# Performance work log

Hardware: AMD Instinct MI355X
Metric: run time of the kernel (lower is better)

Reference implementation:

```python
import jax, jax.numpy as jnp
import numpy as np

# static config (matches init_kwargs)
DIM = 192; NUM_HEAD = 6; HEAD_DIM = DIM // NUM_HEAD
WIN = 8; WS = WIN * WIN            # win_seq = 64
B = 2; H = 256; Wd = 256
RH = H // WIN; RW = Wd // WIN; L = RH * RW   # 32x32 = 1024 windows
P = (2 * WIN - 1) ** 2             # 225 relative positions
SCALE = HEAD_DIM ** -0.5


def _relative_index():
    # same math as get_relative_index (torch.meshgrid default = 'ij')
    coords = np.stack(np.meshgrid(np.arange(WIN), np.arange(WIN), indexing='ij'))
    cf = coords.reshape(2, -1)
    rel = (cf[:, :, None] - cf[:, None, :]).transpose(1, 2, 0).copy()
    rel[:, :, 0] += WIN - 1
    rel[:, :, 1] += WIN - 1
    rel[:, :, 0] *= 2 * WIN - 1
    return rel.sum(-1).reshape(-1)  # (WS*WS,), values in [0, P)

POS_INDEX = jnp.asarray(_relative_index())


def _table_nb(rh, rw):
    # reflect-pad(1) + 3x3 unfold of window-id table -> neighbor window ids (L, 9)
    t = np.arange(rh * rw).reshape(rh, rw)
    tp = np.pad(t, 1, mode='reflect')
    nb = np.stack([tp[kh:kh + rh, kw:kw + rw] for kh in range(3) for kw in range(3)], axis=-1)
    return nb.reshape(rh * rw, 9)

TABLE_NB = jnp.asarray(_table_nb(RH, RW))  # (L, 9) int


def _unfold9(x):
    # x: (B, C, rh, rw) -> (B, L, C, 9); reflect pad 1 + 3x3 neighborhoods
    rh, rw = x.shape[2], x.shape[3]
    xp = jnp.pad(x, ((0, 0), (0, 0), (1, 1), (1, 1)), mode='reflect')
    nb = jnp.stack([xp[:, :, kh:kh + rh, kw:kw + rw] for kh in range(3) for kw in range(3)], axis=-1)
    return nb.reshape(x.shape[0], x.shape[1], rh * rw, 9).transpose(0, 2, 1, 3)


def _router(q, k, pos_embedding):
    # router runs on detached q, k (q.detach() in source)
    qd = jax.lax.stop_gradient(q)
    kd = jax.lax.stop_gradient(k)
    qr = qd.reshape(B, DIM, RH, WIN, RW, WIN).mean(axis=(3, 5))
    kr = kd.reshape(B, DIM, RH, WIN, RW, WIN).mean(axis=(3, 5))
    qr_flat = qr.reshape(B, DIM, L).transpose(0, 2, 1)      # (B, L, C)
    kr_fold = _unfold9(kr)                                   # (B, L, C, 9)
    a_r = jnp.einsum('blc,blcn->bln', qr_flat, kr_fold)      # routing scores
    a_r = a_r.at[..., 4].add(-100.0)                          # exclude self window
    # softmax is monotone -> argmax of a_r equals argmax of softmax(a_r)
    idx = jnp.argmax(a_r, axis=-1)                            # (B, L) in [0,9)
    idx_reflect = TABLE_NB[jnp.arange(L)[None, :], idx]       # (B, L) routed window id
    itself = pos_embedding[4]                                 # (nh, P)
    dirb = pos_embedding[idx]                                 # (B, L, nh, P)
    itself_b = itself[:, POS_INDEX].reshape(NUM_HEAD, WS, WS)
    itself_b = jnp.broadcast_to(itself_b, (B, L, NUM_HEAD, WS, WS))
    dir_b = dirb[..., POS_INDEX].reshape(B, L, NUM_HEAD, WS, WS)
    pos_embed = jnp.concatenate([itself_b, dir_b], axis=-1)   # (B, L, nh, WS, 2*WS)
    return idx_reflect, pos_embed


def reference(x, pos_embedding):
    # x: (B, 3*DIM, H, W) fused qkv feature map
    qc = x[:, :DIM]
    kc = x[:, DIM:2 * DIM]
    idx, pos_embed = _router(qc, kc, pos_embedding)
    # winP: window partition into (3, B, L, nh, WS, hd)
    qkv = x.reshape(B, 3, NUM_HEAD, HEAD_DIM, RH, WIN, RW, WIN)
    qkv = qkv.transpose(1, 0, 4, 6, 2, 5, 7, 3).reshape(3, B, L, NUM_HEAD, WS, HEAD_DIM)
    q, k, v = qkv[0], qkv[1], qkv[2]
    gather = jax.vmap(lambda a, i: a[i])     # per-batch window gather along L
    k_d = gather(k, idx)                     # (B, L, nh, WS, hd)
    v_d = gather(v, idx)
    k_g = jnp.concatenate([k, k_d], axis=3)  # (B, L, nh, 2*WS, hd)
    v_g = jnp.concatenate([v, v_d], axis=3)
    attn = jnp.einsum('blhsd,blhtd->blhst', q, k_g) * SCALE + pos_embed
    attn = jax.nn.softmax(attn, axis=-1)
    out = jnp.einsum('blhst,blhtd->blhsd', attn, v_g)  # (B, L, nh, WS, hd)
    # winR: window reverse to (B, DIM, H, W)
    out = out.reshape(B, RH, RW, NUM_HEAD, WIN, WIN, HEAD_DIM)
    out = out.transpose(0, 3, 6, 1, 4, 2, 5).reshape(B, DIM, H, Wd)
    return out


def setup_inputs() -> dict:
    key = jax.random.key(0)
    k1, k2 = jax.random.split(key)
    x = jax.random.normal(k1, (B, 3 * DIM, H, Wd), dtype=jnp.float32)
    pos_embedding = jax.random.normal(k2, (9, NUM_HEAD, P), dtype=jnp.float32) * 0.02
    return {"x": x, "pos_embedding": pos_embedding}
```

## Files before the change

### kernel.cpp

```cpp
#include <hip/hip_runtime.h>
#include <math.h>

namespace {
constexpr int cB   = 2;
constexpr int cDIM = 192;
constexpr int cNH  = 6;
constexpr int cHD  = 32;
constexpr int cH   = 256;
constexpr int cW   = 256;
constexpr int cRH  = 32;
constexpr int cL   = 1024;
constexpr int cP   = 225;
constexpr float cSCALE = 0.17677669529663688f;
}

typedef _Float16 h8 __attribute__((ext_vector_type(8)));
typedef _Float16 h4 __attribute__((ext_vector_type(4)));
typedef float    f4 __attribute__((ext_vector_type(4)));

__global__ void pool_kernel(const float* __restrict__ x, float* __restrict__ pool) {
    int blk = blockIdx.x;
    int rh = blk & 31;
    int c  = (blk >> 5) % 384;
    int b  = blk / (384 * 32);
    int tid = threadIdx.x;
    int i  = tid >> 5;
    int rw = tid & 31;
    const float* row = x + (((size_t)(b * 576 + c)) * cH + rh * 8 + i) * cW + rw * 8;
    float4 a0 = *(const float4*)row;
    float4 a1 = *(const float4*)(row + 4);
    float s = a0.x + a0.y + a0.z + a0.w + a1.x + a1.y + a1.z + a1.w;
    __shared__ float red[8][33];
    red[i][rw] = s;
    __syncthreads();
    if (tid < 32) {
        float t = 0.f;
        #pragma unroll
        for (int k = 0; k < 8; ++k) t += red[k][tid];
        pool[((size_t)(b * cL) + rh * 32 + tid) * 384 + c] = t * (1.0f / 64.0f);
    }
}

__global__ void router_kernel(const float* __restrict__ pool, int* __restrict__ idxbuf) {
    int blk = blockIdx.x;
    int l = blk & (cL - 1);
    int b = blk >> 10;
    int rh = l >> 5, rw = l & 31;
    int lane = threadIdx.x;
    int ln[9];
    #pragma unroll
    for (int n = 0; n < 9; ++n) {
        int nh = rh + n / 3 - 1;
        int nw = rw + n % 3 - 1;
        nh = nh < 0 ? 1 : (nh > 31 ? 30 : nh);
        nw = nw < 0 ? 1 : (nw > 31 ? 30 : nw);
        ln[n] = nh * 32 + nw;
    }
    float acc[9] = {0,0,0,0,0,0,0,0,0};
    const float* qb = pool + ((size_t)(b * cL) + l) * 384;
    #pragma unroll
    for (int ci = 0; ci < 3; ++ci) {
        int c = lane + ci * 64;
        float q = qb[c];
        #pragma unroll
        for (int n = 0; n < 9; ++n)
            acc[n] += q * pool[((size_t)(b * cL) + ln[n]) * 384 + 192 + c];
    }
    #pragma unroll
    for (int n = 0; n < 9; ++n)
        #pragma unroll
        for (int off = 32; off > 0; off >>= 1)
            acc[n] += __shfl_down(acc[n], off);
    if (lane == 0) {
        acc[4] -= 100.0f;
        int bi = 0; float bv = acc[0];
        #pragma unroll
        for (int n = 1; n < 9; ++n) if (acc[n] > bv) { bv = acc[n]; bi = n; }
        idxbuf[blk * 2]     = bi;
        idxbuf[blk * 2 + 1] = ln[bi];
    }
}

__global__ __launch_bounds__(256, 3) void attn_kernel(
    const float* __restrict__ x, const float* __restrict__ pe,
    const int* __restrict__ idxbuf, float* __restrict__ out)
{
    __shared__ _Float16 Qh[64 * 40];
    __shared__ _Float16 Kh[128 * 40];
    __shared__ _Float16 Vt[32 * 136];
    __shared__ _Float16 Pst[4][16 * 136];
    __shared__ float    pes[2 * cP];

    int blk = blockIdx.x;
    int h  = blk >> 11;
    int bl = blk & 2047;
    int b  = bl >> 10;
    int l  = bl & 1023;
    int rh = l >> 5, rw = l & 31;
    int tid = threadIdx.x;

    int dir  = idxbuf[bl * 2];
    int lwin = idxbuf[bl * 2 + 1];
    int rh2 = lwin >> 5, rw2 = lwin & 31;

    const float* pe_self = pe + (4 * cNH + h) * cP;
    const float* pe_dir  = pe + (dir * cNH + h) * cP;
    for (int t = tid; t < 2 * cP; t += 256)
        pes[t] = (t < cP) ? pe_self[t] : pe_dir[t - cP];

    {
        int d = tid & 31;
        int i = tid >> 5;
        const size_t CHW = (size_t)cH * cW;
        const float* xb = x + (size_t)b * (3 * cDIM) * CHW;
        size_t off_self = (size_t)(rh  * 8 + i) * cW + rw  * 8;
        size_t off_dir  = (size_t)(rh2 * 8 + i) * cW + rw2 * 8;
        size_t cq = (size_t)(h * cHD + d) * CHW;
        size_t ck = cq + (size_t)cDIM * CHW;
        size_t cv = ck + (size_t)cDIM * CHW;

        {
            float4 a0 = *(const float4*)(xb + cq + off_self);
            float4 a1 = *(const float4*)(xb + cq + off_self + 4);
            float vv[8] = {a0.x,a0.y,a0.z,a0.w,a1.x,a1.y,a1.z,a1.w};
            #pragma unroll
            for (int j = 0; j < 8; ++j)
                Qh[(i * 8 + j) * 40 + d] = (_Float16)(vv[j] * cSCALE);
        }
        {
            float4 a0 = *(const float4*)(xb + ck + off_self);
            float4 a1 = *(const float4*)(xb + ck + off_self + 4);
            float vv[8] = {a0.x,a0.y,a0.z,a0.w,a1.x,a1.y,a1.z,a1.w};
            #pragma unroll
            for (int j = 0; j < 8; ++j)
                Kh[(i * 8 + j) * 40 + d] = (_Float16)vv[j];
            float4 b0 = *(const float4*)(xb + ck + off_dir);
            float4 b1 = *(const float4*)(xb + ck + off_dir + 4);
            float ww[8] = {b0.x,b0.y,b0.z,b0.w,b1.x,b1.y,b1.z,b1.w};
            #pragma unroll
            for (int j = 0; j < 8; ++j)
                Kh[(64 + i * 8 + j) * 40 + d] = (_Float16)ww[j];
        }
        {
            float4 a0 = *(const float4*)(xb + cv + off_self);
            float4 a1 = *(const float4*)(xb + cv + off_self + 4);
            h8 hv = { (_Float16)a0.x,(_Float16)a0.y,(_Float16)a0.z,(_Float16)a0.w,
                      (_Float16)a1.x,(_Float16)a1.y,(_Float16)a1.z,(_Float16)a1.w };
            *(h8*)&Vt[d * 136 + i * 8] = hv;
            float4 b0 = *(const float4*)(xb + cv + off_dir);
            float4 b1 = *(const float4*)(xb + cv + off_dir + 4);
            h8 hw = { (_Float16)b0.x,(_Float16)b0.y,(_Float16)b0.z,(_Float16)b0.w,
                      (_Float16)b1.x,(_Float16)b1.y,(_Float16)b1.z,(_Float16)b1.w };
            *(h8*)&Vt[d * 136 + 64 + i * 8] = hw;
        }
    }
    __syncthreads();

    int lane = tid & 63;
    int w    = tid >> 6;
    int g    = lane >> 4;
    int sl   = lane & 15;
    int s_global = w * 16 + sl;

    int base0 = ((s_global >> 3) + 7) * 15 + (s_global & 7) + 7;
    int offs[4];
    #pragma unroll
    for (int q = 0; q < 4; ++q) {
        int gq = 4 * g + q;
        offs[q] = (gq >> 3) * 15 + (gq & 7);
    }

    h8 qf = *(const h8*)&Qh[s_global * 40 + g * 8];
    f4 ST[8];
    #pragma unroll
    for (int T = 0; T < 8; ++T) {
        int base = ((T < 4) ? 0 : cP) + base0 - (T & 3) * 30;
        f4 c;
        #pragma unroll
        for (int q = 0; q < 4; ++q) c[q] = pes[base - offs[q]];
        h8 kf = *(const h8*)&Kh[(T * 16 + sl) * 40 + g * 8];
        ST[T] = __builtin_amdgcn_mfma_f32_16x16x32_f16(kf, qf, c, 0, 0, 0);
    }

    float mx = -1e30f;
    #pragma unroll
    for (int T = 0; T < 8; ++T)
        #pragma unroll
        for (int q = 0; q < 4; ++q) mx = fmaxf(mx, ST[T][q]);
    mx = fmaxf(mx, __shfl_xor(mx, 16));
    mx = fmaxf(mx, __shfl_xor(mx, 32));
    float sum = 0.f;
    #pragma unroll
    for (int T = 0; T < 8; ++T)
        #pragma unroll
        for (int q = 0; q < 4; ++q) { float e = __expf(ST[T][q] - mx); ST[T][q] = e; sum += e; }
    sum += __shfl_xor(sum, 16);
    sum += __shfl_xor(sum, 32);
    float r = 1.0f / sum;

    _Float16* prow = &Pst[w][sl * 136];
    #pragma unroll
    for (int T = 0; T < 8; ++T) {
        h4 p = { (_Float16)(ST[T][0] * r), (_Float16)(ST[T][1] * r),
                 (_Float16)(ST[T][2] * r), (_Float16)(ST[T][3] * r) };
        *(h4*)&prow[T * 16 + g * 4] = p;
    }

    f4 O0 = {0.f,0.f,0.f,0.f}, O1 = {0.f,0.f,0.f,0.f};
    #pragma unroll
    for (int kb = 0; kb < 4; ++kb) {
        h8 pf = *(const h8*)&Pst[w][sl * 136 + kb * 32 + g * 8];
        h8 v0 = *(const h8*)&Vt[ sl       * 136 + kb * 32 + g * 8];
        h8 v1 = *(const h8*)&Vt[(16 + sl) * 136 + kb * 32 + g * 8];
        O0 = __builtin_amdgcn_mfma_f32_16x16x32_f16(v0, pf, O0, 0, 0, 0);
        O1 = __builtin_amdgcn_mfma_f32_16x16x32_f16(v1, pf, O1, 0, 0, 0);
    }

    const size_t CHW = (size_t)cH * cW;
    int pr = rh * 8 + (s_global >> 3);
    int pc = rw * 8 + (s_global & 7);
    float* ob = out + ((size_t)(b * cDIM + h * cHD)) * CHW + (size_t)pr * cW + pc;
    #pragma unroll
    for (int q = 0; q < 4; ++q) {
        ob[(size_t)(4 * g + q) * CHW]      = O0[q];
        ob[(size_t)(16 + 4 * g + q) * CHW] = O1[q];
    }
}

extern "C" void kernel_launch(void* const* d_in, const int* in_sizes, int n_in,
                              void* d_out, int out_size, void* d_ws, size_t ws_size,
                              hipStream_t stream) {
    const float* x  = (const float*)d_in[0];
    const float* pe = (const float*)d_in[1];
    float* out = (float*)d_out;
    float* pool   = (float*)d_ws;
    int*   idxbuf = (int*)((char*)d_ws + (size_t)cB * cL * 384 * sizeof(float));

    hipLaunchKernelGGL(pool_kernel,   dim3(cB * 384 * cRH), dim3(256), 0, stream, x, pool);
    hipLaunchKernelGGL(router_kernel, dim3(cB * cL),        dim3(64),  0, stream, pool, idxbuf);
    hipLaunchKernelGGL(attn_kernel,   dim3(cNH * cB * cL),  dim3(256), 0, stream, x, pe, idxbuf, out);
}
```

Baseline: 610.8 us.

## Pre-transform Q/K/V into per-window fp16 layout fused with pooling

Adds a transform kernel that reads x once, computes the pooled q/k means, and writes Q (pre-scaled), K and V as fp16 in a contiguous per-window, per-head layout. The attention kernel then loads fragments straight from these buffers instead of gathering strided fp32 data from x and staging it in shared memory. This replaces the old separate pool pass and cuts redundant reads of x. The cost is an extra fp16 round trip through global memory of about 3x25MB and a larger workspace. The old path is kept as a fallback for when the workspace is too small.

```diff
diff --git a/kernel.cpp b/kernel.cpp
--- a/kernel.cpp
+++ b/kernel.cpp
@@ -17,6 +17,222 @@
 typedef _Float16 h8 __attribute__((ext_vector_type(8)));
 typedef _Float16 h4 __attribute__((ext_vector_type(4)));
 typedef float    f4 __attribute__((ext_vector_type(4)));
+
+
+__global__ __launch_bounds__(256, 6) void transform_kernel(
+    const float* __restrict__ x, float* __restrict__ pool,
+    _Float16* __restrict__ QT, _Float16* __restrict__ KT, _Float16* __restrict__ VT)
+{
+    __shared__ _Float16 Ls[4 * 64 * 40];
+
+    int blk = blockIdx.x;
+    int rw4 = blk & 7;
+    int rhh = (blk >> 3) & 31;
+    int r   = blk >> 8;
+    int h = r % 6; r /= 6;
+    int t = r % 3;
+    int b = r / 3;
+    int tid  = threadIdx.x;
+    int lane = tid & 63;
+    int hh   = lane >> 3;
+    int ww4  = lane & 7;
+    int c0   = t * cDIM + h * 32;
+    int l0   = rhh * 32 + rw4 * 4;
+
+    const size_t CHW = (size_t)cH * cW;
+    size_t vbase = ((size_t)(b * cNH + h) * cL) * 2048;
+
+    #pragma unroll
+    for (int k = 0; k < 8; ++k) {
+        int c = (tid >> 6) + 4 * k;
+        const float* src = x + ((size_t)(b * 3 * cDIM + c0 + c)) * CHW
+                         + (size_t)(rhh * 8 + hh) * cW + rw4 * 32 + ww4 * 4;
+        float4 v = *(const float4*)src;
+
+        if (t < 2) {
+            float ps = v.x + v.y + v.z + v.w;
+            ps += __shfl_xor(ps, 1);
+            ps += __shfl_xor(ps, 8);
+            ps += __shfl_xor(ps, 16);
+            ps += __shfl_xor(ps, 32);
+            if ((lane & 1) == 0 && lane < 8) {
+                int w = lane >> 1;
+                pool[((size_t)(b * cL) + l0 + w) * 384 + t * 192 + h * 32 + c] = ps * (1.0f / 64.0f);
+            }
+            float sc = (t == 0) ? cSCALE : 1.0f;
+            int ll = ww4 >> 1;
+            int s0 = hh * 8 + (ww4 & 1) * 4;
+            float vv[4] = {v.x, v.y, v.z, v.w};
+            #pragma unroll
+            for (int j = 0; j < 4; ++j)
+                Ls[(ll * 64 + s0 + j) * 40 + c] = (_Float16)(vv[j] * sc);
+        } else {
+            int ll = ww4 >> 1;
+            int tt = hh * 8 + (ww4 & 1) * 4;
+            h4 hv = { (_Float16)v.x, (_Float16)v.y, (_Float16)v.z, (_Float16)v.w };
+            *(h4*)&VT[vbase + (size_t)(l0 + ll) * 2048 + c * 64 + tt] = hv;
+        }
+    }
+
+    if (t < 2) {
+        __syncthreads();
+        _Float16* dst = (t == 0) ? QT : KT;
+        size_t obase = ((size_t)(b * cNH + h) * cL) * 2048;
+        #pragma unroll
+        for (int j = 0; j < 4; ++j) {
+            int linear = tid + 256 * j;
+            int ll = linear >> 8;
+            int s  = (linear >> 2) & 63;
+            int d8 = linear & 3;
+            h8 val = *(const h8*)&Ls[(ll * 64 + s) * 40 + d8 * 8];
+            *(h8*)&dst[obase + (size_t)(l0 + ll) * 2048 + s * 32 + d8 * 8] = val;
+        }
+    }
+}
+
+__global__ void router_kernel(const float* __restrict__ pool, int* __restrict__ idxbuf) {
+    int blk = blockIdx.x;
+    int l = blk & (cL - 1);
+    int b = blk >> 10;
+    int rh = l >> 5, rw = l & 31;
+    int lane = threadIdx.x;
+    int ln[9];
+    #pragma unroll
+    for (int n = 0; n < 9; ++n) {
+        int nh = rh + n / 3 - 1;
+        int nw = rw + n % 3 - 1;
+        nh = nh < 0 ? 1 : (nh > 31 ? 30 : nh);
+        nw = nw < 0 ? 1 : (nw > 31 ? 30 : nw);
+        ln[n] = nh * 32 + nw;
+    }
+    float acc[9] = {0,0,0,0,0,0,0,0,0};
+    const float* qb = pool + ((size_t)(b * cL) + l) * 384;
+    #pragma unroll
+    for (int ci = 0; ci < 3; ++ci) {
+        int c = lane + ci * 64;
+        float q = qb[c];
+        #pragma unroll
+        for (int n = 0; n < 9; ++n)
+            acc[n] += q * pool[((size_t)(b * cL) + ln[n]) * 384 + 192 + c];
+    }
+    #pragma unroll
+    for (int n = 0; n < 9; ++n)
+        #pragma unroll
+        for (int off = 32; off > 0; off >>= 1)
+            acc[n] += __shfl_down(acc[n], off);
+    if (lane == 0) {
+        acc[4] -= 100.0f;
+        int bi = 0; float bv = acc[0];
+        #pragma unroll
+        for (int n = 1; n < 9; ++n) if (acc[n] > bv) { bv = acc[n]; bi = n; }
+        idxbuf[blk * 2]     = bi;
+        idxbuf[blk * 2 + 1] = ln[bi];
+    }
+}
+
+__global__ __launch_bounds__(256, 5) void attn_kernel(
+    const _Float16* __restrict__ QT, const _Float16* __restrict__ KT,
+    const _Float16* __restrict__ VT, const float* __restrict__ pe,
+    const int* __restrict__ idxbuf, float* __restrict__ out)
+{
+    __shared__ float    pes[2 * cP];
+    __shared__ _Float16 Pst[4][16 * 136];
+
+    int blk = blockIdx.x;
+    int h  = blk >> 11;
+    int bl = blk & 2047;
+    int b  = bl >> 10;
+    int l  = bl & 1023;
+    int rh = l >> 5, rw = l & 31;
+    int tid = threadIdx.x;
+
+    int dir  = idxbuf[bl * 2];
+    int lwin = idxbuf[bl * 2 + 1];
+
+    const float* pe_self = pe + (4 * cNH + h) * cP;
+    const float* pe_dir  = pe + (dir * cNH + h) * cP;
+    for (int tt = tid; tt < 2 * cP; tt += 256)
+        pes[tt] = (tt < cP) ? pe_self[tt] : pe_dir[tt - cP];
+    __syncthreads();
+
+    int lane = tid & 63;
+    int w    = tid >> 6;
+    int g    = lane >> 4;
+    int sl   = lane & 15;
+    int s_global = w * 16 + sl;
+
+    size_t base  = ((size_t)(b * cNH + h) * cL + l)    * 2048;
+    size_t baseD = ((size_t)(b * cNH + h) * cL + lwin) * 2048;
+
+    int base0 = ((s_global >> 3) + 7) * 15 + (s_global & 7) + 7;
+    int offs[4];
+    #pragma unroll
+    for (int q = 0; q < 4; ++q) {
+        int gq = 4 * g + q;
+        offs[q] = (gq >> 3) * 15 + (gq & 7);
+    }
+
+    h8 qf = *(const h8*)&QT[base + s_global * 32 + g * 8];
+    f4 ST[8];
+    #pragma unroll
+    for (int T = 0; T < 8; ++T) {
+        int bias = ((T < 4) ? 0 : cP) + base0 - (T & 3) * 30;
+        f4 c;
+        #pragma unroll
+        for (int q = 0; q < 4; ++q) c[q] = pes[bias - offs[q]];
+        h8 kf = (T < 4)
+            ? *(const h8*)&KT[base  + (T * 16 + sl) * 32 + g * 8]
+            : *(const h8*)&KT[baseD + ((T - 4) * 16 + sl) * 32 + g * 8];
+        ST[T] = __builtin_amdgcn_mfma_f32_16x16x32_f16(kf, qf, c, 0, 0, 0);
+    }
+
+    float mx = -1e30f;
+    #pragma unroll
+    for (int T = 0; T < 8; ++T)
+        #pragma unroll
+        for (int q = 0; q < 4; ++q) mx = fmaxf(mx, ST[T][q]);
+    mx = fmaxf(mx, __shfl_xor(mx, 16));
+    mx = fmaxf(mx, __shfl_xor(mx, 32));
+    float sum = 0.f;
+    #pragma unroll
+    for (int T = 0; T < 8; ++T)
+        #pragma unroll
+        for (int q = 0; q < 4; ++q) { float e = __expf(ST[T][q] - mx); ST[T][q] = e; sum += e; }
+    sum += __shfl_xor(sum, 16);
+    sum += __shfl_xor(sum, 32);
+    float r = 1.0f / sum;
+
+    _Float16* prow = &Pst[w][sl * 136];
+    #pragma unroll
+    for (int T = 0; T < 8; ++T) {
+        h4 p = { (_Float16)(ST[T][0] * r), (_Float16)(ST[T][1] * r),
+                 (_Float16)(ST[T][2] * r), (_Float16)(ST[T][3] * r) };
+        *(h4*)&prow[T * 16 + g * 4] = p;
+    }
+
+    f4 O0 = {0.f,0.f,0.f,0.f}, O1 = {0.f,0.f,0.f,0.f};
+    #pragma unroll
+    for (int kb = 0; kb < 4; ++kb) {
+        h8 pf = *(const h8*)&Pst[w][sl * 136 + kb * 32 + g * 8];
+        size_t vb = (kb < 2) ? (base  + (kb * 32 + g * 8))
+                             : (baseD + ((kb - 2) * 32 + g * 8));
+        h8 v0 = *(const h8*)&VT[vb + sl * 64];
+        h8 v1 = *(const h8*)&VT[vb + (16 + sl) * 64];
+        O0 = __builtin_amdgcn_mfma_f32_16x16x32_f16(v0, pf, O0, 0, 0, 0);
+        O1 = __builtin_amdgcn_mfma_f32_16x16x32_f16(v1, pf, O1, 0, 0, 0);
+    }
+
+    const size_t CHW = (size_t)cH * cW;
+    int pr = rh * 8 + (s_global >> 3);
+    int pc = rw * 8 + (s_global & 7);
+    float* ob = out + ((size_t)(b * cDIM + h * cHD)) * CHW + (size_t)pr * cW + pc;
+    #pragma unroll
+    for (int q = 0; q < 4; ++q) {
+        ob[(size_t)(4 * g + q) * CHW]      = O0[q];
+        ob[(size_t)(16 + 4 * g + q) * CHW] = O1[q];
+    }
+}
+
 
 __global__ void pool_kernel(const float* __restrict__ x, float* __restrict__ pool) {
     int blk = blockIdx.x;
@@ -41,47 +257,7 @@
     }
 }
 
-__global__ void router_kernel(const float* __restrict__ pool, int* __restrict__ idxbuf) {
-    int blk = blockIdx.x;
-    int l = blk & (cL - 1);
-    int b = blk >> 10;
-    int rh = l >> 5, rw = l & 31;
-    int lane = threadIdx.x;
-    int ln[9];
-    #pragma unroll
-    for (int n = 0; n < 9; ++n) {
-        int nh = rh + n / 3 - 1;
-        int nw = rw + n % 3 - 1;
-        nh = nh < 0 ? 1 : (nh > 31 ? 30 : nh);
-        nw = nw < 0 ? 1 : (nw > 31 ? 30 : nw);
-        ln[n] = nh * 32 + nw;
-    }
-    float acc[9] = {0,0,0,0,0,0,0,0,0};
-    const float* qb = pool + ((size_t)(b * cL) + l) * 384;
-    #pragma unroll
-    for (int ci = 0; ci < 3; ++ci) {
-        int c = lane + ci * 64;
-        float q = qb[c];
-        #pragma unroll
-        for (int n = 0; n < 9; ++n)
-            acc[n] += q * pool[((size_t)(b * cL) + ln[n]) * 384 + 192 + c];
-    }
-    #pragma unroll
-    for (int n = 0; n < 9; ++n)
-        #pragma unroll
-        for (int off = 32; off > 0; off >>= 1)
-            acc[n] += __shfl_down(acc[n], off);
-    if (lane == 0) {
-        acc[4] -= 100.0f;
-        int bi = 0; float bv = acc[0];
-        #pragma unroll
-        for (int n = 1; n < 9; ++n) if (acc[n] > bv) { bv = acc[n]; bi = n; }
-        idxbuf[blk * 2]     = bi;
-        idxbuf[blk * 2 + 1] = ln[bi];
-    }
-}
-
-__global__ __launch_bounds__(256, 3) void attn_kernel(
+__global__ __launch_bounds__(256, 3) void attn_old_kernel(
     const float* __restrict__ x, const float* __restrict__ pe,
     const int* __restrict__ idxbuf, float* __restrict__ out)
 {
@@ -118,28 +294,24 @@
         size_t cq = (size_t)(h * cHD + d) * CHW;
         size_t ck = cq + (size_t)cDIM * CHW;
         size_t cv = ck + (size_t)cDIM * CHW;
-
         {
             float4 a0 = *(const float4*)(xb + cq + off_self);
             float4 a1 = *(const float4*)(xb + cq + off_self + 4);
             float vv[8] = {a0.x,a0.y,a0.z,a0.w,a1.x,a1.y,a1.z,a1.w};
             #pragma unroll
-            for (int j = 0; j < 8; ++j)
-                Qh[(i * 8 + j) * 40 + d] = (_Float16)(vv[j] * cSCALE);
+            for (int j = 0; j < 8; ++j) Qh[(i * 8 + j) * 40 + d] = (_Float16)(vv[j] * cSCALE);
         }
         {
             float4 a0 = *(const float4*)(xb + ck + off_self);
             float4 a1 = *(const float4*)(xb + ck + off_self + 4);
             float vv[8] = {a0.x,a0.y,a0.z,a0.w,a1.x,a1.y,a1.z,a1.w};
             #pragma unroll
-            for (int j = 0; j < 8; ++j)
-                Kh[(i * 8 + j) * 40 + d] = (_Float16)vv[j];
+            for (int j = 0; j < 8; ++j) Kh[(i * 8 + j) * 40 + d] = (_Float16)vv[j];
             float4 b0 = *(const float4*)(xb + ck + off_dir);
             float4 b1 = *(const float4*)(xb + ck + off_dir + 4);
             float ww[8] = {b0.x,b0.y,b0.z,b0.w,b1.x,b1.y,b1.z,b1.w};
             #pragma unroll
-            for (int j = 0; j < 8; ++j)
-                Kh[(64 + i * 8 + j) * 40 + d] = (_Float16)ww[j];
+            for (int j = 0; j < 8; ++j) Kh[(64 + i * 8 + j) * 40 + d] = (_Float16)ww[j];
         }
         {
             float4 a0 = *(const float4*)(xb + cv + off_self);
@@ -174,10 +346,10 @@
     f4 ST[8];
     #pragma unroll
     for (int T = 0; T < 8; ++T) {
-        int base = ((T < 4) ? 0 : cP) + base0 - (T & 3) * 30;
+        int bias = ((T < 4) ? 0 : cP) + base0 - (T & 3) * 30;
         f4 c;
         #pragma unroll
-        for (int q = 0; q < 4; ++q) c[q] = pes[base - offs[q]];
+        for (int q = 0; q < 4; ++q) c[q] = pes[bias - offs[q]];
         h8 kf = *(const h8*)&Kh[(T * 16 + sl) * 40 + g * 8];
         ST[T] = __builtin_amdgcn_mfma_f32_16x16x32_f16(kf, qf, c, 0, 0, 0);
     }
@@ -227,16 +399,37 @@
     }
 }
 
+
 extern "C" void kernel_launch(void* const* d_in, const int* in_sizes, int n_in,
                               void* d_out, int out_size, void* d_ws, size_t ws_size,
                               hipStream_t stream) {
     const float* x  = (const float*)d_in[0];
     const float* pe = (const float*)d_in[1];
     float* out = (float*)d_out;
-    float* pool   = (float*)d_ws;
-    int*   idxbuf = (int*)((char*)d_ws + (size_t)cB * cL * 384 * sizeof(float));
-
-    hipLaunchKernelGGL(pool_kernel,   dim3(cB * 384 * cRH), dim3(256), 0, stream, x, pool);
-    hipLaunchKernelGGL(router_kernel, dim3(cB * cL),        dim3(64),  0, stream, pool, idxbuf);
-    hipLaunchKernelGGL(attn_kernel,   dim3(cNH * cB * cL),  dim3(256), 0, stream, x, pe, idxbuf, out);
-}
+
+    const size_t OFF_POOL = 0;
+    const size_t OFF_IDX  = (size_t)cB * cL * 384 * sizeof(float);
+    const size_t OFF_QT   = OFF_IDX + 16384;
+    const size_t SZ_T     = (size_t)cB * cNH * cL * 2048 * sizeof(_Float16);
+    const size_t OFF_KT   = OFF_QT + SZ_T;
+    const size_t OFF_VT   = OFF_KT + SZ_T;
+    const size_t NEED     = OFF_VT + SZ_T;
+
+    float* pool   = (float*)((char*)d_ws + OFF_POOL);
+    int*   idxbuf = (int*)((char*)d_ws + OFF_IDX);
+
+    if (ws_size >= NEED) {
+        _Float16* QT = (_Float16*)((char*)d_ws + OFF_QT);
+        _Float16* KT = (_Float16*)((char*)d_ws + OFF_KT);
+        _Float16* VT = (_Float16*)((char*)d_ws + OFF_VT);
+        hipLaunchKernelGGL(transform_kernel, dim3(cB * 3 * cNH * cRH * 8), dim3(256), 0, stream,
+                           x, pool, QT, KT, VT);
+        hipLaunchKernelGGL(router_kernel,    dim3(cB * cL),  dim3(64),  0, stream, pool, idxbuf);
+        hipLaunchKernelGGL(attn_kernel,      dim3(cNH * cB * cL), dim3(256), 0, stream,
+                           QT, KT, VT, pe, idxbuf, out);
+    } else {
+        hipLaunchKernelGGL(pool_kernel,     dim3(cB * 384 * cRH), dim3(256), 0, stream, x, pool);
+        hipLaunchKernelGGL(router_kernel,   dim3(cB * cL),        dim3(64),  0, stream, pool, idxbuf);
+        hipLaunchKernelGGL(attn_old_kernel, dim3(cNH * cB * cL),  dim3(256), 0, stream, x, pe, idxbuf, out);
+    }
+}
```

After: 552.9 us. 1.1x faster.
